# Kernel optimization log

Hardware: AMD Instinct MI355X
Metric: run time of the kernel (lower is better)

The kernel has to match this reference:

```python
import jax, jax.numpy as jnp
import numpy as np

WIN = 8
SHIFT = 4
HEADS = 4


def _relative_position_index(w: int) -> np.ndarray:
    coords = np.stack(np.meshgrid(np.arange(w), np.arange(w), indexing='ij'))  # [2,w,w]
    coords = coords.reshape(2, -1)                                             # [2,w*w]
    rel = coords[:, :, None] - coords[:, None, :]                              # [2,N,N]
    rel = rel.transpose(1, 2, 0).copy()                                        # [N,N,2]
    rel[:, :, 0] += w - 1
    rel[:, :, 1] += w - 1
    rel[:, :, 0] *= 2 * w - 1
    return rel.sum(-1)                                                         # [N,N]

_REL_IDX = _relative_position_index(WIN)


def setup_inputs() -> dict:
    key = jax.random.key(0)
    ks = jax.random.split(key, 6)
    C = 128
    return {
        'x': jax.random.normal(ks[0], (4, 512, 512, C), dtype=jnp.float32),
        'qkv_w': jax.random.normal(ks[1], (C, 3 * C), dtype=jnp.float32) * 0.02,
        'qkv_b': jax.random.normal(ks[2], (3 * C,), dtype=jnp.float32) * 0.02,
        'proj_w': jax.random.normal(ks[3], (C, C), dtype=jnp.float32) * 0.02,
        'proj_b': jax.random.normal(ks[4], (C,), dtype=jnp.float32) * 0.02,
        'bias_table': jax.random.normal(ks[5], ((2 * WIN - 1) ** 2, HEADS), dtype=jnp.float32) * 0.02,
    }


def reference(x, qkv_w, qkv_b, proj_w, proj_b, bias_table):
    B, H, W, C = x.shape
    w = WIN
    heads = HEADS
    hd = C // heads
    scale = hd ** -0.5
    N = w * w

    # cyclic shift
    if SHIFT > 0:
        x = jnp.roll(x, (-SHIFT, -SHIFT), axis=(1, 2))

    # pad spatial dims to multiples of w (no-op for divisible shapes)
    pH = (w - H % w) % w
    pW = (w - W % w) % w
    if pH or pW:
        x = jnp.pad(x, ((0, 0), (0, pH), (0, pW), (0, 0)))
    Hp, Wp = H + pH, W + pW
    nH, nW = Hp // w, Wp // w

    # window partition -> [B*nH*nW, N, C]
    xw = x.reshape(B, nH, w, nW, w, C).transpose(0, 1, 3, 2, 4, 5).reshape(B * nH * nW, N, C)

    # QKV projection
    qkv = xw @ qkv_w + qkv_b                                  # [nw, N, 3C]
    qkv = qkv.reshape(-1, N, 3, heads, hd).transpose(2, 0, 3, 1, 4)  # [3, nw, h, N, hd]
    q, k, v = qkv[0], qkv[1], qkv[2]

    # attention with relative position bias
    attn = jnp.einsum('bhnd,bhmd->bhnm', q, k) * scale        # [nw, h, N, N]
    bias = bias_table[_REL_IDX.reshape(-1)].reshape(N, N, heads).transpose(2, 0, 1)
    attn = jax.nn.softmax(attn + bias[None], axis=-1)
    out = jnp.einsum('bhnm,bhmd->bhnd', attn, v)              # [nw, h, N, hd]
    out = out.transpose(0, 2, 1, 3).reshape(-1, N, C)

    # output projection
    out = out @ proj_w + proj_b

    # window reverse + unpad
    out = out.reshape(B, nH, nW, w, w, C).transpose(0, 1, 3, 2, 4, 5).reshape(B, Hp, Wp, C)
    out = out[:, :H, :W, :]

    if SHIFT > 0:
        out = jnp.roll(out, (SHIFT, SHIFT), axis=(1, 2))
    return out
```

## Files before the change

kernel.cpp:

```cpp
#include <hip/hip_runtime.h>

#define IMG 512
#define CCH 128
#define NHEAD 4
#define HDIM 32
#define NTOK 64
#define SHIFT_AMT 4

typedef __attribute__((ext_vector_type(8))) short bf16x8;
typedef __attribute__((ext_vector_type(4))) short short4v;
typedef __attribute__((ext_vector_type(4))) float f32x4;

__device__ __forceinline__ short f2bf(float f) {
    unsigned u = __float_as_uint(f);
    unsigned r = (u + 0x7FFFu + ((u >> 16) & 1u)) >> 16;
    return (short)r;
}

__global__ __launch_bounds__(256)
void cvt_weights(const float* __restrict__ qkv_w, const float* __restrict__ proj_w,
                 short* __restrict__ wqkvt, short* __restrict__ wpt)
{
    int idx = blockIdx.x * 256 + threadIdx.x;
    if (idx < 384 * 128) {
        int n = idx >> 7, k = idx & 127;
        wqkvt[idx] = f2bf(qkv_w[k * 384 + n]);
    } else {
        int i2 = idx - 384 * 128;
        int n = i2 >> 7, k = i2 & 127;
        wpt[i2] = f2bf(proj_w[k * 128 + n]);
    }
}

__global__ __launch_bounds__(256, 2)
void win_attn_mfma(const float* __restrict__ x,
                   const short* __restrict__ wqkvt,
                   const float* __restrict__ qkv_b,
                   const short* __restrict__ wpt,
                   const float* __restrict__ proj_b,
                   const float* __restrict__ bias_table,
                   float* __restrict__ out)
{
    __shared__ __align__(16) short qs[NTOK][136];
    __shared__ __align__(16) short ks[NTOK][136];
    __shared__ __align__(16) short vt[CCH][72];
    __shared__ __align__(16) short ps[NTOK][72];

    const int tid  = threadIdx.x;
    const int wv   = tid >> 6;
    const int lane = tid & 63;
    const int l16  = lane & 15;
    const int q16  = lane >> 4;

    const int widx = blockIdx.x;
    const int b  = widx >> 12;
    const int wh = (widx >> 6) & 63;
    const int ww = widx & 63;

    const f32x4 zf = {0.f, 0.f, 0.f, 0.f};

    size_t pixoff[4];
    #pragma unroll
    for (int mt = 0; mt < 4; ++mt) {
        const int tok = mt * 16 + l16;
        const int hh_ = (wh * 8 + (tok >> 3) + SHIFT_AMT) & (IMG - 1);
        const int ww_ = (ww * 8 + (tok & 7)  + SHIFT_AMT) & (IMG - 1);
        pixoff[mt] = (((size_t)b * IMG + hh_) * IMG + ww_) * CCH;
    }

    f32x4 acc1[6][4];
    #pragma unroll
    for (int nt = 0; nt < 6; ++nt)
        #pragma unroll
        for (int mt = 0; mt < 4; ++mt) acc1[nt][mt] = zf;

    #pragma unroll
    for (int kk = 0; kk < 4; ++kk) {
        bf16x8 a[4];
        #pragma unroll
        for (int mt = 0; mt < 4; ++mt) {
            const float* p = x + pixoff[mt] + kk * 32 + q16 * 8;
            const float4 f0 = *(const float4*)p;
            const float4 f1 = *(const float4*)(p + 4);
            bf16x8 av;
            av[0] = f2bf(f0.x); av[1] = f2bf(f0.y); av[2] = f2bf(f0.z); av[3] = f2bf(f0.w);
            av[4] = f2bf(f1.x); av[5] = f2bf(f1.y); av[6] = f2bf(f1.z); av[7] = f2bf(f1.w);
            a[mt] = av;
        }
        #pragma unroll
        for (int nt = 0; nt < 6; ++nt) {
            const short* wp = wqkvt + (size_t)(wv * 96 + nt * 16 + l16) * 128 + kk * 32 + q16 * 8;
            const bf16x8 bfr = *(const bf16x8*)wp;
            #pragma unroll
            for (int mt = 0; mt < 4; ++mt)
                acc1[nt][mt] = __builtin_amdgcn_mfma_f32_16x16x32_bf16(a[mt], bfr, acc1[nt][mt], 0, 0, 0);
        }
    }

    #pragma unroll
    for (int nt = 0; nt < 6; ++nt) {
        const int n0  = wv * 96 + nt * 16;
        const int col = n0 + l16;
        const float bias = qkv_b[col];
        if (n0 < 128) {
            #pragma unroll
            for (int mt = 0; mt < 4; ++mt)
                #pragma unroll
                for (int r = 0; r < 4; ++r)
                    qs[mt * 16 + q16 * 4 + r][col] = f2bf(acc1[nt][mt][r] + bias);
        } else if (n0 < 256) {
            #pragma unroll
            for (int mt = 0; mt < 4; ++mt)
                #pragma unroll
                for (int r = 0; r < 4; ++r)
                    ks[mt * 16 + q16 * 4 + r][col - 128] = f2bf(acc1[nt][mt][r] + bias);
        } else {
            #pragma unroll
            for (int mt = 0; mt < 4; ++mt) {
                short4v pk;
                pk[0] = f2bf(acc1[nt][mt][0] + bias);
                pk[1] = f2bf(acc1[nt][mt][1] + bias);
                pk[2] = f2bf(acc1[nt][mt][2] + bias);
                pk[3] = f2bf(acc1[nt][mt][3] + bias);
                *(short4v*)&vt[col - 256][mt * 16 + q16 * 4] = pk;
            }
        }
    }
    __syncthreads();

    const float scale = 0.17677669529663687f;
    f32x4 oacc[8];
    #pragma unroll
    for (int i = 0; i < 8; ++i) oacc[i] = zf;

    const int qrow_base = wv * 16 + q16 * 4;

    #pragma unroll
    for (int h = 0; h < NHEAD; ++h) {
        const bf16x8 aq = *(const bf16x8*)&qs[wv * 16 + l16][h * 32 + q16 * 8];
        f32x4 s[4];
        #pragma unroll
        for (int nt = 0; nt < 4; ++nt) {
            const bf16x8 bk = *(const bf16x8*)&ks[nt * 16 + l16][h * 32 + q16 * 8];
            s[nt] = __builtin_amdgcn_mfma_f32_16x16x32_bf16(aq, bk, zf, 0, 0, 0);
        }
        #pragma unroll
        for (int r = 0; r < 4; ++r) {
            const int qrow = qrow_base + r;
            const int qi = qrow >> 3, qj = qrow & 7;
            #pragma unroll
            for (int nt = 0; nt < 4; ++nt) {
                const int kn = nt * 16 + l16;
                const int rel = (qi - (kn >> 3) + 7) * 15 + (qj - (kn & 7) + 7);
                s[nt][r] = s[nt][r] * scale + bias_table[rel * NHEAD + h];
            }
            float mx = fmaxf(fmaxf(s[0][r], s[1][r]), fmaxf(s[2][r], s[3][r]));
            mx = fmaxf(mx, __shfl_xor(mx, 1));
            mx = fmaxf(mx, __shfl_xor(mx, 2));
            mx = fmaxf(mx, __shfl_xor(mx, 4));
            mx = fmaxf(mx, __shfl_xor(mx, 8));
            float sum = 0.f;
            #pragma unroll
            for (int nt = 0; nt < 4; ++nt) { s[nt][r] = __expf(s[nt][r] - mx); sum += s[nt][r]; }
            sum += __shfl_xor(sum, 1);
            sum += __shfl_xor(sum, 2);
            sum += __shfl_xor(sum, 4);
            sum += __shfl_xor(sum, 8);
            const float inv = 1.f / sum;
            #pragma unroll
            for (int nt = 0; nt < 4; ++nt) s[nt][r] *= inv;
        }
        #pragma unroll
        for (int nt = 0; nt < 4; ++nt)
            #pragma unroll
            for (int r = 0; r < 4; ++r)
                ps[qrow_base + r][nt * 16 + l16] = f2bf(s[nt][r]);

        #pragma unroll
        for (int kk = 0; kk < 2; ++kk) {
            const bf16x8 ap = *(const bf16x8*)&ps[wv * 16 + l16][kk * 32 + q16 * 8];
            #pragma unroll
            for (int ntv = 0; ntv < 2; ++ntv) {
                const bf16x8 bv = *(const bf16x8*)&vt[h * 32 + ntv * 16 + l16][kk * 32 + q16 * 8];
                oacc[h * 2 + ntv] = __builtin_amdgcn_mfma_f32_16x16x32_bf16(ap, bv, oacc[h * 2 + ntv], 0, 0, 0);
            }
        }
    }

    __syncthreads();
    short (*os)[136] = qs;
    #pragma unroll
    for (int h = 0; h < NHEAD; ++h)
        #pragma unroll
        for (int ntv = 0; ntv < 2; ++ntv)
            #pragma unroll
            for (int r = 0; r < 4; ++r)
                os[qrow_base + r][h * 32 + ntv * 16 + l16] = f2bf(oacc[h * 2 + ntv][r]);
    __syncthreads();

    f32x4 c2[2][4];
    #pragma unroll
    for (int nt = 0; nt < 2; ++nt)
        #pragma unroll
        for (int mt = 0; mt < 4; ++mt) c2[nt][mt] = zf;

    #pragma unroll
    for (int kk = 0; kk < 4; ++kk) {
        bf16x8 am[4];
        #pragma unroll
        for (int mt = 0; mt < 4; ++mt)
            am[mt] = *(const bf16x8*)&os[mt * 16 + l16][kk * 32 + q16 * 8];
        #pragma unroll
        for (int nt = 0; nt < 2; ++nt) {
            const short* wp = wpt + (size_t)(wv * 32 + nt * 16 + l16) * 128 + kk * 32 + q16 * 8;
            const bf16x8 bw = *(const bf16x8*)wp;
            #pragma unroll
            for (int mt = 0; mt < 4; ++mt)
                c2[nt][mt] = __builtin_amdgcn_mfma_f32_16x16x32_bf16(am[mt], bw, c2[nt][mt], 0, 0, 0);
        }
    }

    #pragma unroll
    for (int nt = 0; nt < 2; ++nt) {
        const int col = wv * 32 + nt * 16 + l16;
        const float pb = proj_b[col];
        #pragma unroll
        for (int mt = 0; mt < 4; ++mt) {
            #pragma unroll
            for (int r = 0; r < 4; ++r) {
                const int tok = mt * 16 + q16 * 4 + r;
                const int hh_ = (wh * 8 + (tok >> 3) + SHIFT_AMT) & (IMG - 1);
                const int ww_ = (ww * 8 + (tok & 7)  + SHIFT_AMT) & (IMG - 1);
                out[(((size_t)b * IMG + hh_) * IMG + ww_) * CCH + col] = c2[nt][mt][r] + pb;
            }
        }
    }
}

extern "C" void kernel_launch(void* const* d_in, const int* in_sizes, int n_in,
                              void* d_out, int out_size, void* d_ws, size_t ws_size,
                              hipStream_t stream)
{
    const float* x        = (const float*)d_in[0];
    const float* qkv_w    = (const float*)d_in[1];
    const float* qkv_b    = (const float*)d_in[2];
    const float* proj_w   = (const float*)d_in[3];
    const float* proj_b   = (const float*)d_in[4];
    const float* bias_tab = (const float*)d_in[5];
    float* out = (float*)d_out;

    short* wqkvt = (short*)d_ws;
    short* wpt   = wqkvt + 384 * 128;

    hipLaunchKernelGGL(cvt_weights, dim3(256), dim3(256), 0, stream,
                       qkv_w, proj_w, wqkvt, wpt);
    hipLaunchKernelGGL(win_attn_mfma, dim3(4 * 64 * 64), dim3(256), 0, stream,
                       x, wqkvt, qkv_b, wpt, proj_b, bias_tab, out);
}
```

Baseline: 1.397 ms.

## Rework window attention with transposed MFMA, register-resident P/O, swizzled LDS

Precomputes the dense per-head relative-position bias matrix in the weight-conversion kernel and reads it directly instead of gathering through the index table. The attention is recomputed transposed (keys as A operand), so the softmax reduction needs only two cross-lane shuffles. P and the attention output now stay in registers and are redistributed with lane shuffles, which removes the ps buffer, the extra LDS round trip and two barriers. The change also swaps padded LDS rows for XOR-swizzled ones, uses hardware packed bf16 conversion, folds biases into accumulator init and raises the occupancy hint to 3. LDS use shrinks but register pressure and shuffle count go up.

```diff
diff --git a/kernel.cpp b/kernel.cpp
--- a/kernel.cpp
+++ b/kernel.cpp
@@ -3,13 +3,21 @@
 #define IMG 512
 #define CCH 128
 #define NHEAD 4
-#define HDIM 32
 #define NTOK 64
 #define SHIFT_AMT 4
 
 typedef __attribute__((ext_vector_type(8))) short bf16x8;
-typedef __attribute__((ext_vector_type(4))) short short4v;
 typedef __attribute__((ext_vector_type(4))) float f32x4;
+typedef __attribute__((ext_vector_type(4))) unsigned int u32x4;
+typedef __attribute__((ext_vector_type(2))) unsigned int u32x2;
+
+union BF8 { u32x4 u; bf16x8 b; };
+
+__device__ __forceinline__ unsigned cvtpk(float lo, float hi) {
+    unsigned r;
+    asm("v_cvt_pk_bf16_f32 %0, %1, %2" : "=v"(r) : "v"(lo), "v"(hi));
+    return r;
+}
 
 __device__ __forceinline__ short f2bf(float f) {
     unsigned u = __float_as_uint(f);
@@ -19,32 +27,37 @@
 
 __global__ __launch_bounds__(256)
 void cvt_weights(const float* __restrict__ qkv_w, const float* __restrict__ proj_w,
-                 short* __restrict__ wqkvt, short* __restrict__ wpt)
+                 const float* __restrict__ bias_table,
+                 short* __restrict__ wqkvt, short* __restrict__ wpt, float* __restrict__ biasM)
 {
     int idx = blockIdx.x * 256 + threadIdx.x;
     if (idx < 384 * 128) {
         int n = idx >> 7, k = idx & 127;
         wqkvt[idx] = f2bf(qkv_w[k * 384 + n]);
-    } else {
+    } else if (idx < 384 * 128 + 128 * 128) {
         int i2 = idx - 384 * 128;
         int n = i2 >> 7, k = i2 & 127;
         wpt[i2] = f2bf(proj_w[k * 128 + n]);
-    }
-}
-
-__global__ __launch_bounds__(256, 2)
+    } else {
+        int i3 = idx - (384 * 128 + 128 * 128);
+        int h = i3 >> 12, key = (i3 >> 6) & 63, q = i3 & 63;
+        int rel = ((q >> 3) - (key >> 3) + 7) * 15 + ((q & 7) - (key & 7) + 7);
+        biasM[i3] = bias_table[rel * NHEAD + h];
+    }
+}
+
+__global__ __launch_bounds__(256, 3)
 void win_attn_mfma(const float* __restrict__ x,
                    const short* __restrict__ wqkvt,
                    const float* __restrict__ qkv_b,
                    const short* __restrict__ wpt,
                    const float* __restrict__ proj_b,
-                   const float* __restrict__ bias_table,
+                   const float* __restrict__ biasM,
                    float* __restrict__ out)
 {
-    __shared__ __align__(16) short qs[NTOK][136];
-    __shared__ __align__(16) short ks[NTOK][136];
-    __shared__ __align__(16) short vt[CCH][72];
-    __shared__ __align__(16) short ps[NTOK][72];
+    __shared__ __align__(16) short qs[NTOK * CCH];
+    __shared__ __align__(16) short ks[NTOK * CCH];
+    __shared__ __align__(16) short vt[CCH * NTOK];
 
     const int tid  = threadIdx.x;
     const int wv   = tid >> 6;
@@ -59,41 +72,42 @@
 
     const f32x4 zf = {0.f, 0.f, 0.f, 0.f};
 
-    size_t pixoff[4];
+    unsigned xoff[4];
     #pragma unroll
     for (int mt = 0; mt < 4; ++mt) {
         const int tok = mt * 16 + l16;
         const int hh_ = (wh * 8 + (tok >> 3) + SHIFT_AMT) & (IMG - 1);
         const int ww_ = (ww * 8 + (tok & 7)  + SHIFT_AMT) & (IMG - 1);
-        pixoff[mt] = (((size_t)b * IMG + hh_) * IMG + ww_) * CCH;
+        xoff[mt] = (((unsigned)b * IMG + hh_) * IMG + ww_) * CCH;
     }
 
     f32x4 acc1[6][4];
     #pragma unroll
-    for (int nt = 0; nt < 6; ++nt)
-        #pragma unroll
-        for (int mt = 0; mt < 4; ++mt) acc1[nt][mt] = zf;
+    for (int nt = 0; nt < 6; ++nt) {
+        const float bv = qkv_b[wv * 96 + nt * 16 + l16];
+        #pragma unroll
+        for (int mt = 0; mt < 4; ++mt) acc1[nt][mt] = (f32x4){bv, bv, bv, bv};
+    }
 
     #pragma unroll
     for (int kk = 0; kk < 4; ++kk) {
         bf16x8 a[4];
         #pragma unroll
         for (int mt = 0; mt < 4; ++mt) {
-            const float* p = x + pixoff[mt] + kk * 32 + q16 * 8;
+            const float* p = x + xoff[mt] + kk * 32 + q16 * 8;
             const float4 f0 = *(const float4*)p;
             const float4 f1 = *(const float4*)(p + 4);
-            bf16x8 av;
-            av[0] = f2bf(f0.x); av[1] = f2bf(f0.y); av[2] = f2bf(f0.z); av[3] = f2bf(f0.w);
-            av[4] = f2bf(f1.x); av[5] = f2bf(f1.y); av[6] = f2bf(f1.z); av[7] = f2bf(f1.w);
-            a[mt] = av;
+            BF8 cv;
+            cv.u = (u32x4){cvtpk(f0.x, f0.y), cvtpk(f0.z, f0.w),
+                           cvtpk(f1.x, f1.y), cvtpk(f1.z, f1.w)};
+            a[mt] = cv.b;
         }
         #pragma unroll
         for (int nt = 0; nt < 6; ++nt) {
-            const short* wp = wqkvt + (size_t)(wv * 96 + nt * 16 + l16) * 128 + kk * 32 + q16 * 8;
-            const bf16x8 bfr = *(const bf16x8*)wp;
+            const bf16x8 bw = *(const bf16x8*)(wqkvt + (wv * 96 + nt * 16 + l16) * 128 + kk * 32 + q16 * 8);
             #pragma unroll
             for (int mt = 0; mt < 4; ++mt)
-                acc1[nt][mt] = __builtin_amdgcn_mfma_f32_16x16x32_bf16(a[mt], bfr, acc1[nt][mt], 0, 0, 0);
+                acc1[nt][mt] = __builtin_amdgcn_mfma_f32_16x16x32_bf16(a[mt], bw, acc1[nt][mt], 0, 0, 0);
         }
     }
 
@@ -101,139 +115,131 @@
     for (int nt = 0; nt < 6; ++nt) {
         const int n0  = wv * 96 + nt * 16;
         const int col = n0 + l16;
-        const float bias = qkv_b[col];
-        if (n0 < 128) {
-            #pragma unroll
-            for (int mt = 0; mt < 4; ++mt)
-                #pragma unroll
-                for (int r = 0; r < 4; ++r)
-                    qs[mt * 16 + q16 * 4 + r][col] = f2bf(acc1[nt][mt][r] + bias);
-        } else if (n0 < 256) {
-            #pragma unroll
-            for (int mt = 0; mt < 4; ++mt)
-                #pragma unroll
-                for (int r = 0; r < 4; ++r)
-                    ks[mt * 16 + q16 * 4 + r][col - 128] = f2bf(acc1[nt][mt][r] + bias);
-        } else {
-            #pragma unroll
-            for (int mt = 0; mt < 4; ++mt) {
-                short4v pk;
-                pk[0] = f2bf(acc1[nt][mt][0] + bias);
-                pk[1] = f2bf(acc1[nt][mt][1] + bias);
-                pk[2] = f2bf(acc1[nt][mt][2] + bias);
-                pk[3] = f2bf(acc1[nt][mt][3] + bias);
-                *(short4v*)&vt[col - 256][mt * 16 + q16 * 4] = pk;
+        #pragma unroll
+        for (int mt = 0; mt < 4; ++mt) {
+            const unsigned p01 = cvtpk(acc1[nt][mt][0], acc1[nt][mt][1]);
+            const unsigned p23 = cvtpk(acc1[nt][mt][2], acc1[nt][mt][3]);
+            const int t0 = mt * 16 + q16 * 4;
+            if (n0 < 128) {
+                qs[(t0+0)*CCH + (col ^ (((t0+0)&7)<<3))] = (short)(p01 & 0xFFFFu);
+                qs[(t0+1)*CCH + (col ^ (((t0+1)&7)<<3))] = (short)(p01 >> 16);
+                qs[(t0+2)*CCH + (col ^ (((t0+2)&7)<<3))] = (short)(p23 & 0xFFFFu);
+                qs[(t0+3)*CCH + (col ^ (((t0+3)&7)<<3))] = (short)(p23 >> 16);
+            } else if (n0 < 256) {
+                const int kc = col - 128;
+                ks[(t0+0)*CCH + (kc ^ (((t0+0)&7)<<3))] = (short)(p01 & 0xFFFFu);
+                ks[(t0+1)*CCH + (kc ^ (((t0+1)&7)<<3))] = (short)(p01 >> 16);
+                ks[(t0+2)*CCH + (kc ^ (((t0+2)&7)<<3))] = (short)(p23 & 0xFFFFu);
+                ks[(t0+3)*CCH + (kc ^ (((t0+3)&7)<<3))] = (short)(p23 >> 16);
+            } else {
+                const int ch = col - 256;
+                u32x2 pk2 = {p01, p23};
+                *(u32x2*)&vt[ch * NTOK + (t0 ^ ((ch & 7) << 3))] = pk2;
             }
         }
     }
     __syncthreads();
 
+    const int myA = l16 + ((lane & 16) << 1);
+    const int myB = myA + 16;
+    const bool hiq = (lane >= 32);
+    const int qrow = wv * 16 + l16;
     const float scale = 0.17677669529663687f;
-    f32x4 oacc[8];
-    #pragma unroll
-    for (int i = 0; i < 8; ++i) oacc[i] = zf;
-
-    const int qrow_base = wv * 16 + q16 * 4;
+    const float* bM = biasM + q16 * 256 + qrow;
+
+    unsigned ok[16];
 
     #pragma unroll
     for (int h = 0; h < NHEAD; ++h) {
-        const bf16x8 aq = *(const bf16x8*)&qs[wv * 16 + l16][h * 32 + q16 * 8];
+        const bf16x8 bq = *(const bf16x8*)&qs[qrow * CCH + ((h*32 + q16*8) ^ ((qrow & 7) << 3))];
         f32x4 s[4];
         #pragma unroll
         for (int nt = 0; nt < 4; ++nt) {
-            const bf16x8 bk = *(const bf16x8*)&ks[nt * 16 + l16][h * 32 + q16 * 8];
-            s[nt] = __builtin_amdgcn_mfma_f32_16x16x32_bf16(aq, bk, zf, 0, 0, 0);
-        }
-        #pragma unroll
-        for (int r = 0; r < 4; ++r) {
-            const int qrow = qrow_base + r;
-            const int qi = qrow >> 3, qj = qrow & 7;
-            #pragma unroll
-            for (int nt = 0; nt < 4; ++nt) {
-                const int kn = nt * 16 + l16;
-                const int rel = (qi - (kn >> 3) + 7) * 15 + (qj - (kn & 7) + 7);
-                s[nt][r] = s[nt][r] * scale + bias_table[rel * NHEAD + h];
-            }
-            float mx = fmaxf(fmaxf(s[0][r], s[1][r]), fmaxf(s[2][r], s[3][r]));
-            mx = fmaxf(mx, __shfl_xor(mx, 1));
-            mx = fmaxf(mx, __shfl_xor(mx, 2));
-            mx = fmaxf(mx, __shfl_xor(mx, 4));
-            mx = fmaxf(mx, __shfl_xor(mx, 8));
-            float sum = 0.f;
-            #pragma unroll
-            for (int nt = 0; nt < 4; ++nt) { s[nt][r] = __expf(s[nt][r] - mx); sum += s[nt][r]; }
-            sum += __shfl_xor(sum, 1);
-            sum += __shfl_xor(sum, 2);
-            sum += __shfl_xor(sum, 4);
-            sum += __shfl_xor(sum, 8);
-            const float inv = 1.f / sum;
-            #pragma unroll
-            for (int nt = 0; nt < 4; ++nt) s[nt][r] *= inv;
-        }
+            const int krow = nt * 16 + l16;
+            const bf16x8 ak = *(const bf16x8*)&ks[krow * CCH + ((h*32 + q16*8) ^ ((krow & 7) << 3))];
+            s[nt] = __builtin_amdgcn_mfma_f32_16x16x32_bf16(ak, bq, zf, 0, 0, 0);
+        }
+        float mx = -3.0e38f;
         #pragma unroll
         for (int nt = 0; nt < 4; ++nt)
             #pragma unroll
-            for (int r = 0; r < 4; ++r)
-                ps[qrow_base + r][nt * 16 + l16] = f2bf(s[nt][r]);
-
-        #pragma unroll
-        for (int kk = 0; kk < 2; ++kk) {
-            const bf16x8 ap = *(const bf16x8*)&ps[wv * 16 + l16][kk * 32 + q16 * 8];
-            #pragma unroll
-            for (int ntv = 0; ntv < 2; ++ntv) {
-                const bf16x8 bv = *(const bf16x8*)&vt[h * 32 + ntv * 16 + l16][kk * 32 + q16 * 8];
-                oacc[h * 2 + ntv] = __builtin_amdgcn_mfma_f32_16x16x32_bf16(ap, bv, oacc[h * 2 + ntv], 0, 0, 0);
+            for (int r = 0; r < 4; ++r) {
+                s[nt][r] = s[nt][r] * scale + bM[h*4096 + nt*1024 + r*64];
+                mx = fmaxf(mx, s[nt][r]);
             }
-        }
-    }
-
-    __syncthreads();
-    short (*os)[136] = qs;
-    #pragma unroll
-    for (int h = 0; h < NHEAD; ++h)
-        #pragma unroll
-        for (int ntv = 0; ntv < 2; ++ntv)
-            #pragma unroll
-            for (int r = 0; r < 4; ++r)
-                os[qrow_base + r][h * 32 + ntv * 16 + l16] = f2bf(oacc[h * 2 + ntv][r]);
-    __syncthreads();
-
-    f32x4 c2[2][4];
-    #pragma unroll
-    for (int nt = 0; nt < 2; ++nt)
-        #pragma unroll
-        for (int mt = 0; mt < 4; ++mt) c2[nt][mt] = zf;
-
-    #pragma unroll
-    for (int kk = 0; kk < 4; ++kk) {
-        bf16x8 am[4];
-        #pragma unroll
-        for (int mt = 0; mt < 4; ++mt)
-            am[mt] = *(const bf16x8*)&os[mt * 16 + l16][kk * 32 + q16 * 8];
-        #pragma unroll
-        for (int nt = 0; nt < 2; ++nt) {
-            const short* wp = wpt + (size_t)(wv * 32 + nt * 16 + l16) * 128 + kk * 32 + q16 * 8;
-            const bf16x8 bw = *(const bf16x8*)wp;
-            #pragma unroll
-            for (int mt = 0; mt < 4; ++mt)
-                c2[nt][mt] = __builtin_amdgcn_mfma_f32_16x16x32_bf16(am[mt], bw, c2[nt][mt], 0, 0, 0);
-        }
-    }
-
-    #pragma unroll
-    for (int nt = 0; nt < 2; ++nt) {
-        const int col = wv * 32 + nt * 16 + l16;
-        const float pb = proj_b[col];
-        #pragma unroll
-        for (int mt = 0; mt < 4; ++mt) {
+        mx = fmaxf(mx, __shfl_xor(mx, 16));
+        mx = fmaxf(mx, __shfl_xor(mx, 32));
+        float sum = 0.f;
+        #pragma unroll
+        for (int nt = 0; nt < 4; ++nt)
             #pragma unroll
             for (int r = 0; r < 4; ++r) {
-                const int tok = mt * 16 + q16 * 4 + r;
-                const int hh_ = (wh * 8 + (tok >> 3) + SHIFT_AMT) & (IMG - 1);
-                const int ww_ = (ww * 8 + (tok & 7)  + SHIFT_AMT) & (IMG - 1);
-                out[(((size_t)b * IMG + hh_) * IMG + ww_) * CCH + col] = c2[nt][mt][r] + pb;
+                s[nt][r] = __expf(s[nt][r] - mx);
+                sum += s[nt][r];
             }
-        }
+        sum += __shfl_xor(sum, 16);
+        sum += __shfl_xor(sum, 32);
+        const float inv = 1.f / sum;
+
+        unsigned pkf[8];
+        #pragma unroll
+        for (int nt = 0; nt < 4; ++nt) {
+            pkf[nt*2+0] = cvtpk(s[nt][0], s[nt][1]);
+            pkf[nt*2+1] = cvtpk(s[nt][2], s[nt][3]);
+        }
+
+        f32x4 o0 = zf, o1 = zf;
+        #pragma unroll
+        for (int kk = 0; kk < 2; ++kk) {
+            const unsigned a0 = __shfl(pkf[4*kk+0], myA), b0 = __shfl(pkf[4*kk+2], myA);
+            const unsigned a1 = __shfl(pkf[4*kk+1], myA), b1 = __shfl(pkf[4*kk+3], myA);
+            const unsigned a2 = __shfl(pkf[4*kk+0], myB), b2 = __shfl(pkf[4*kk+2], myB);
+            const unsigned a3 = __shfl(pkf[4*kk+1], myB), b3 = __shfl(pkf[4*kk+3], myB);
+            BF8 bp;
+            bp.u = (u32x4){hiq ? b0 : a0, hiq ? b1 : a1, hiq ? b2 : a2, hiq ? b3 : a3};
+            const int c0 = h * 32 + l16;
+            const int c1 = c0 + 16;
+            const bf16x8 av0 = *(const bf16x8*)&vt[c0 * NTOK + ((kk*32 + q16*8) ^ ((c0 & 7) << 3))];
+            const bf16x8 av1 = *(const bf16x8*)&vt[c1 * NTOK + ((kk*32 + q16*8) ^ ((c1 & 7) << 3))];
+            o0 = __builtin_amdgcn_mfma_f32_16x16x32_bf16(av0, bp.b, o0, 0, 0, 0);
+            o1 = __builtin_amdgcn_mfma_f32_16x16x32_bf16(av1, bp.b, o1, 0, 0, 0);
+        }
+        ok[h*4+0] = cvtpk(o0[0]*inv, o0[1]*inv);
+        ok[h*4+1] = cvtpk(o0[2]*inv, o0[3]*inv);
+        ok[h*4+2] = cvtpk(o1[0]*inv, o1[1]*inv);
+        ok[h*4+3] = cvtpk(o1[2]*inv, o1[3]*inv);
+    }
+
+    f32x4 c2[8];
+    #pragma unroll
+    for (int nt = 0; nt < 8; ++nt) {
+        const float pb = proj_b[nt * 16 + l16];
+        c2[nt] = (f32x4){pb, pb, pb, pb};
+    }
+
+    #pragma unroll
+    for (int kk = 0; kk < 4; ++kk) {
+        const unsigned a0 = __shfl(ok[4*kk+0], myA), b0 = __shfl(ok[4*kk+2], myA);
+        const unsigned a1 = __shfl(ok[4*kk+1], myA), b1 = __shfl(ok[4*kk+3], myA);
+        const unsigned a2 = __shfl(ok[4*kk+0], myB), b2 = __shfl(ok[4*kk+2], myB);
+        const unsigned a3 = __shfl(ok[4*kk+1], myB), b3 = __shfl(ok[4*kk+3], myB);
+        BF8 am;
+        am.u = (u32x4){hiq ? b0 : a0, hiq ? b1 : a1, hiq ? b2 : a2, hiq ? b3 : a3};
+        #pragma unroll
+        for (int nt = 0; nt < 8; ++nt) {
+            const bf16x8 bw = *(const bf16x8*)(wpt + (nt * 16 + l16) * 128 + kk * 32 + q16 * 8);
+            c2[nt] = __builtin_amdgcn_mfma_f32_16x16x32_bf16(am.b, bw, c2[nt], 0, 0, 0);
+        }
+    }
+
+    const int hh_ = (wh * 8 + 2 * wv + (q16 >> 1) + SHIFT_AMT) & (IMG - 1);
+    const unsigned wbase = ww * 8 + 4 * (q16 & 1) + SHIFT_AMT;
+    #pragma unroll
+    for (int r = 0; r < 4; ++r) {
+        const int ww_ = (wbase + r) & (IMG - 1);
+        float* po = out + (((unsigned)b * IMG + hh_) * IMG + ww_) * CCH + l16;
+        #pragma unroll
+        for (int nt = 0; nt < 8; ++nt) po[nt * 16] = c2[nt][r];
     }
 }
 
@@ -251,9 +257,10 @@
 
     short* wqkvt = (short*)d_ws;
     short* wpt   = wqkvt + 384 * 128;
-
-    hipLaunchKernelGGL(cvt_weights, dim3(256), dim3(256), 0, stream,
-                       qkv_w, proj_w, wqkvt, wpt);
+    float* biasM = (float*)((char*)d_ws + 131072);
+
+    hipLaunchKernelGGL(cvt_weights, dim3(320), dim3(256), 0, stream,
+                       qkv_w, proj_w, bias_tab, wqkvt, wpt, biasM);
     hipLaunchKernelGGL(win_attn_mfma, dim3(4 * 64 * 64), dim3(256), 0, stream,
-                       x, wqkvt, qkv_b, wpt, proj_b, bias_tab, out);
-}
+                       x, wqkvt, qkv_b, wpt, proj_b, biasM, out);
+}
```

Result: no change. 1.396 ms (-0.1%).
